# Performance work log

Hardware: AMD Instinct MI355X
Metric: run time of the kernel (lower is better)

Reference implementation:

```python
import jax, jax.numpy as jnp
import numpy as np

T, E, H, K = 8192, 512, 512, 19  # seq_len, embed_dim, per-direction hidden, tagset
START, STOP, NEG = 17, 18, -10000.0


def _lstm_dir(x, w_ih, w_hh, b_ih, b_hh, h0, c0):
    # x: [T, E]; PyTorch gate order i, f, g, o. Precompute input contribution.
    xg = x @ w_ih.T + b_ih + b_hh  # [T, 4H]

    def step(carry, xg_t):
        h, c = carry
        g = xg_t + h @ w_hh.T
        i, f, gg, o = jnp.split(g, 4)
        c = jax.nn.sigmoid(f) * c + jax.nn.sigmoid(i) * jnp.tanh(gg)
        h = jax.nn.sigmoid(o) * jnp.tanh(c)
        return (h, c), h

    _, hs = jax.lax.scan(step, (h0, c0), xg)
    return hs  # [T, H]


def setup_inputs() -> dict:
    key = jax.random.key(0)
    ks = jax.random.split(key, 16)
    s = 0.05
    trans = jax.random.normal(ks[13], (K, K), jnp.float32)
    trans = trans.at[START, :].set(NEG)  # never transition into START
    trans = trans.at[:, STOP].set(NEG)   # never transition from STOP
    return {
        "sentence": jax.random.normal(ks[0], (T, 1, E), jnp.float32),
        "w_ih_f": jax.random.normal(ks[1], (4 * H, E), jnp.float32) * s,
        "w_hh_f": jax.random.normal(ks[2], (4 * H, H), jnp.float32) * s,
        "b_ih_f": jax.random.normal(ks[3], (4 * H,), jnp.float32) * s,
        "b_hh_f": jax.random.normal(ks[4], (4 * H,), jnp.float32) * s,
        "w_ih_b": jax.random.normal(ks[5], (4 * H, E), jnp.float32) * s,
        "w_hh_b": jax.random.normal(ks[6], (4 * H, H), jnp.float32) * s,
        "b_ih_b": jax.random.normal(ks[7], (4 * H,), jnp.float32) * s,
        "b_hh_b": jax.random.normal(ks[8], (4 * H,), jnp.float32) * s,
        "h0": jax.random.normal(ks[9], (2, 1, H), jnp.float32),
        "c0": jax.random.normal(ks[10], (2, 1, H), jnp.float32),
        "W_tag": jax.random.normal(ks[11], (K, 2 * H), jnp.float32) * s,
        "b_tag": jax.random.normal(ks[12], (K,), jnp.float32) * s,
        "transitions": trans,
    }


def reference(sentence, w_ih_f, w_hh_f, b_ih_f, b_hh_f, w_ih_b, w_hh_b, b_ih_b, b_hh_b, h0, c0, W_tag, b_tag, transitions):
    x = sentence[:, 0, :]  # [T, E], batch = 1
    hs_f = _lstm_dir(x, w_ih_f, w_hh_f, b_ih_f, b_hh_f, h0[0, 0], c0[0, 0])
    hs_b = _lstm_dir(x[::-1], w_ih_b, w_hh_b, b_ih_b, b_hh_b, h0[1, 0], c0[1, 0])[::-1]
    lstm_out = jnp.concatenate([hs_f, hs_b], axis=-1)  # [T, 2H]
    feats = lstm_out @ W_tag.T + b_tag  # [T, K] emission scores

    # Viterbi decode: transitions[i, j] = score of j -> i
    init = jnp.full((K,), NEG, jnp.float32).at[START].set(0.0)

    def vstep(fv, feat):
        nt = fv[None, :] + transitions      # [K, K]
        bptr = jnp.argmax(nt, axis=1)       # best previous tag per current tag
        fv_new = jnp.max(nt, axis=1) + feat
        return fv_new, bptr

    fv, bptrs = jax.lax.scan(vstep, init, feats)  # bptrs: [T, K]
    terminal = fv + transitions[STOP]
    best = jnp.argmax(terminal)
    path_score = terminal[best]

    def back(tag, bptr):
        return bptr[tag], tag

    _, best_path = jax.lax.scan(back, best, bptrs, reverse=True)  # [T]
    return path_score, best_path
```

## Files before the change

kernel.cpp:

```cpp
#include <hip/hip_runtime.h>
#include <hip/hip_fp16.h>

#define T_LEN 8192
#define E_DIM 512
#define H_DIM 512
#define G4    2048
#define KTAGS 19
#define START_TAG 17
#define STOP_TAG  18
#define NEGV  (-10000.0f)
#define VCH   64
#define VCL   128
#define LSTM_LDS ((16384 + 256 + 1024 + 64) * 4)

typedef _Float16 h2v __attribute__((ext_vector_type(2)));
union HU { unsigned int u; h2v h; };

__device__ __forceinline__ float sigf_(float x) {
  x = fminf(fmaxf(x, -30.f), 30.f);
  return 1.f / (1.f + __expf(-x));
}
__device__ __forceinline__ float tanhf_(float x) {
  x = fminf(fmaxf(x, -15.f), 15.f);
  const float e = __expf(2.f * x);
  return (e - 1.f) / (e + 1.f);
}

__device__ __forceinline__ unsigned int pack2(float a, float b) {
  HU u; u.h.x = (_Float16)a; u.h.y = (_Float16)b; return u.u;
}

__device__ __forceinline__ float dot2f(unsigned int a, unsigned int b, float acc) {
#if __has_builtin(__builtin_amdgcn_fdot2)
  HU ua; ua.u = a; HU ub; ub.u = b;
  return __builtin_amdgcn_fdot2(ua.h, ub.h, acc, false);
#else
  HU ua; ua.u = a; HU ub; ub.u = b;
  return acc + (float)ua.h.x * (float)ub.h.x + (float)ua.h.y * (float)ub.h.y;
#endif
}

__global__ __launch_bounds__(256) void k_xg(
    const float* __restrict__ x,
    const float* __restrict__ wih_f, const float* __restrict__ bih_f, const float* __restrict__ bhh_f,
    const float* __restrict__ wih_b, const float* __restrict__ bih_b, const float* __restrict__ bhh_b,
    __half* __restrict__ xg_out)
{
  const int dir = blockIdx.z;
  const float* __restrict__ wih = dir ? wih_b : wih_f;
  const float* __restrict__ bih = dir ? bih_b : bih_f;
  const float* __restrict__ bhh = dir ? bhh_b : bhh_f;
  __shared__ float xs[16][68];
  __shared__ float wsd[16][68];
  const int tid = threadIdx.x;
  const int tm = tid >> 4, tn = tid & 15;
  const int m0 = blockIdx.y * 64, n0 = blockIdx.x * 64;
  const int lr = tid >> 2;
  const int lk = (tid & 3) << 2;
  float acc[4][4] = {{0.f,0.f,0.f,0.f},{0.f,0.f,0.f,0.f},{0.f,0.f,0.f,0.f},{0.f,0.f,0.f,0.f}};
  for (int k0 = 0; k0 < E_DIM; k0 += 16) {
    const int gm = m0 + lr;
    const int xrow = dir ? (T_LEN - 1 - gm) : gm;
    const float4 xa = *reinterpret_cast<const float4*>(&x[(size_t)xrow * E_DIM + k0 + lk]);
    const float4 wa = *reinterpret_cast<const float4*>(&wih[(size_t)(n0 + lr) * E_DIM + k0 + lk]);
    __syncthreads();
    xs[lk+0][lr] = xa.x; xs[lk+1][lr] = xa.y; xs[lk+2][lr] = xa.z; xs[lk+3][lr] = xa.w;
    wsd[lk+0][lr] = wa.x; wsd[lk+1][lr] = wa.y; wsd[lk+2][lr] = wa.z; wsd[lk+3][lr] = wa.w;
    __syncthreads();
    #pragma unroll
    for (int kk = 0; kk < 16; ++kk) {
      const float4 a = *reinterpret_cast<const float4*>(&xs[kk][tm << 2]);
      const float4 b = *reinterpret_cast<const float4*>(&wsd[kk][tn << 2]);
      acc[0][0] += a.x*b.x; acc[0][1] += a.x*b.y; acc[0][2] += a.x*b.z; acc[0][3] += a.x*b.w;
      acc[1][0] += a.y*b.x; acc[1][1] += a.y*b.y; acc[1][2] += a.y*b.z; acc[1][3] += a.y*b.w;
      acc[2][0] += a.z*b.x; acc[2][1] += a.z*b.y; acc[2][2] += a.z*b.z; acc[2][3] += a.z*b.w;
      acc[3][0] += a.w*b.x; acc[3][1] += a.w*b.y; acc[3][2] += a.w*b.z; acc[3][3] += a.w*b.w;
    }
  }
  const int n = n0 + (tn << 2);
  float4 bb;
  bb.x = bih[n+0] + bhh[n+0];
  bb.y = bih[n+1] + bhh[n+1];
  bb.z = bih[n+2] + bhh[n+2];
  bb.w = bih[n+3] + bhh[n+3];
  __half* o = xg_out + (size_t)dir * T_LEN * G4;
  #pragma unroll
  for (int mi = 0; mi < 4; ++mi) {
    const size_t base = (size_t)(m0 + (tm << 2) + mi) * G4 + n;
    unsigned int p0 = pack2(acc[mi][0] + bb.x, acc[mi][1] + bb.y);
    unsigned int p1 = pack2(acc[mi][2] + bb.z, acc[mi][3] + bb.w);
    uint2 st; st.x = p0; st.y = p1;
    *reinterpret_cast<uint2*>(&o[base]) = st;
  }
}

__global__ __launch_bounds__(512, 1) void k_lstm(
    const float* __restrict__ whh_f, const float* __restrict__ whh_b,
    const float* __restrict__ h0, const float* __restrict__ c0,
    const __half* __restrict__ xg_base, unsigned long long* __restrict__ hht)
{
  const int b = blockIdx.x;
  if ((b & 7) >= 2) return;
  const int dir = b & 7;
  const int idx = b >> 3;
  const float* __restrict__ whh = dir ? whh_b : whh_f;
  const __half* xg16 = xg_base + (size_t)dir * T_LEN * G4;
  unsigned long long* hp = hht + (size_t)dir * T_LEN * 256;

  extern __shared__ unsigned int lds[];
  unsigned int* wl  = lds;
  unsigned int* hlb = lds + 16384;
  float* pgl        = (float*)(lds + 16384 + 256);

  const int tid = threadIdx.x;
  const int w = tid >> 6, l = tid & 63;
  const int gate = l >> 4, j = l & 15;
  const int H0 = idx * 16;
  const int Rrow = gate * H_DIM + H0 + j;

  {
    const float4* src = reinterpret_cast<const float4*>(&whh[(size_t)Rrow * H_DIM + (w << 6)]);
    #pragma unroll
    for (int m = 0; m < 8; ++m) {
      const float4 a = src[2*m], d = src[2*m+1];
      uint4 pk;
      pk.x = pack2(a.x, a.y); pk.y = pack2(a.z, a.w);
      pk.z = pack2(d.x, d.y); pk.w = pack2(d.z, d.w);
      *reinterpret_cast<uint4*>(&wl[(((w << 3) + m) * 64 + l) * 4]) = pk;
    }
  }
  const uint4* wb = reinterpret_cast<const uint4*>(wl) + ((w << 3) * 64 + l);
  uint4 w0 = wb[0*64], w1 = wb[1*64], w2 = wb[2*64], w3 = wb[3*64],
        w4 = wb[4*64], w5 = wb[5*64], w6 = wb[6*64], w7 = wb[7*64];

  float cstate = 0.f;
  if (w == 0 && l < 16) cstate = c0[dir * H_DIM + H0 + l];
  float xcur = 0.f, xnext = 0.f;
  if (w == 0) {
    xcur  = __half2float(xg16[Rrow]);
    xnext = __half2float(xg16[(size_t)G4 + Rrow]);
  }

  for (int t = 0; t < T_LEN; ++t) {
    const int buf = t & 1;
    if (l < 32) {
      const int pw = (w << 5) + l;
      unsigned int pair;
      if (t > 0) {
        const unsigned long long* src = &hp[(size_t)(t - 1) * 256 + pw];
        unsigned long long v = __hip_atomic_load(src, __ATOMIC_RELAXED, __HIP_MEMORY_SCOPE_AGENT);
        while ((unsigned)(v >> 32) != (unsigned)t)
          v = __hip_atomic_load(src, __ATOMIC_RELAXED, __HIP_MEMORY_SCOPE_AGENT);
        pair = (unsigned)v;
      } else {
        pair = pack2(h0[dir * H_DIM + 2 * pw], h0[dir * H_DIM + 2 * pw + 1]);
      }
      hlb[pw] = pair;
    }
    const uint4* hb = reinterpret_cast<const uint4*>(&hlb[w << 5]);
    float acc0 = 0.f, acc1 = 0.f;
    uint4 hv;
    hv = hb[0];
    acc0 = dot2f(w0.x, hv.x, acc0); acc1 = dot2f(w0.y, hv.y, acc1);
    acc0 = dot2f(w0.z, hv.z, acc0); acc1 = dot2f(w0.w, hv.w, acc1);
    hv = hb[1];
    acc0 = dot2f(w1.x, hv.x, acc0); acc1 = dot2f(w1.y, hv.y, acc1);
    acc0 = dot2f(w1.z, hv.z, acc0); acc1 = dot2f(w1.w, hv.w, acc1);
    hv = hb[2];
    acc0 = dot2f(w2.x, hv.x, acc0); acc1 = dot2f(w2.y, hv.y, acc1);
    acc0 = dot2f(w2.z, hv.z, acc0); acc1 = dot2f(w2.w, hv.w, acc1);
    hv = hb[3];
    acc0 = dot2f(w3.x, hv.x, acc0); acc1 = dot2f(w3.y, hv.y, acc1);
    acc0 = dot2f(w3.z, hv.z, acc0); acc1 = dot2f(w3.w, hv.w, acc1);
    hv = hb[4];
    acc0 = dot2f(w4.x, hv.x, acc0); acc1 = dot2f(w4.y, hv.y, acc1);
    acc0 = dot2f(w4.z, hv.z, acc0); acc1 = dot2f(w4.w, hv.w, acc1);
    hv = hb[5];
    acc0 = dot2f(w5.x, hv.x, acc0); acc1 = dot2f(w5.y, hv.y, acc1);
    acc0 = dot2f(w5.z, hv.z, acc0); acc1 = dot2f(w5.w, hv.w, acc1);
    hv = hb[6];
    acc0 = dot2f(w6.x, hv.x, acc0); acc1 = dot2f(w6.y, hv.y, acc1);
    acc0 = dot2f(w6.z, hv.z, acc0); acc1 = dot2f(w6.w, hv.w, acc1);
    hv = hb[7];
    acc0 = dot2f(w7.x, hv.x, acc0); acc1 = dot2f(w7.y, hv.y, acc1);
    acc0 = dot2f(w7.z, hv.z, acc0); acc1 = dot2f(w7.w, hv.w, acc1);
    pgl[buf * 512 + (w << 6) + l] = acc0 + acc1;
    __syncthreads();

    if (w == 0) {
      const float* pb = &pgl[buf * 512 + l];
      const float tr = pb[0] + pb[64] + pb[128] + pb[192]
                     + pb[256] + pb[320] + pb[384] + pb[448];
      const float gv = tr + xcur;
      const bool isg = (gate == 2);
      const float sarg = isg ? 2.f * gv : gv;
      const float sg = sigf_(sarg);
      const float p = isg ? 2.f * sg - 1.f : sg;
      const float pi  = __shfl(p, j, 64);
      const float pf  = __shfl(p, 16 + j, 64);
      const float pgv = __shfl(p, 32 + j, 64);
      const float po  = __shfl(p, 48 + j, 64);
      float hval = 0.f;
      if (l < 16) {
        cstate = pf * cstate + pi * pgv;
        hval = po * tanhf_(cstate);
      }
      const float hop = __shfl(hval, l + 1, 64);
      if (l < 16 && (l & 1) == 0) {
        const unsigned long long pv =
            (unsigned long long)pack2(hval, hop) | ((unsigned long long)(t + 1) << 32);
        __hip_atomic_store(&hp[(size_t)t * 256 + idx * 8 + (l >> 1)], pv,
                           __ATOMIC_RELAXED, __HIP_MEMORY_SCOPE_AGENT);
      }
      xcur = xnext;
      xnext = (t + 2 < T_LEN) ? __half2float(xg16[(size_t)(t + 2) * G4 + Rrow]) : 0.f;
    }
  }
}

__global__ __launch_bounds__(64) void k_feats(
    const unsigned long long* __restrict__ hht, const float* __restrict__ Wtag,
    const float* __restrict__ btag, float* __restrict__ feats)
{
  const int t = blockIdx.x;
  const int tid = threadIdx.x;
  __shared__ float hbuf[1024];
  const unsigned long long* hfp = hht + (size_t)t * 256;
  const unsigned long long* hbp = hht + (size_t)T_LEN * 256 + (size_t)(T_LEN - 1 - t) * 256;
  for (int m = tid; m < 256; m += 64) {
    HU u; u.u = (unsigned)hfp[m];
    hbuf[2*m] = (float)u.h.x; hbuf[2*m+1] = (float)u.h.y;
    HU v; v.u = (unsigned)hbp[m];
    hbuf[512 + 2*m] = (float)v.h.x; hbuf[512 + 2*m+1] = (float)v.h.y;
  }
  __syncthreads();
  const int k = tid;
  if (k >= KTAGS) return;
  const float* wr = &Wtag[(size_t)k * 1024];
  float acc = btag[k];
  #pragma unroll 4
  for (int d = 0; d < 256; ++d) {
    const float4 h4 = *reinterpret_cast<const float4*>(&hbuf[4 * d]);
    const float4 w4 = *reinterpret_cast<const float4*>(&wr[4 * d]);
    acc += h4.x*w4.x + h4.y*w4.y + h4.z*w4.z + h4.w*w4.w;
  }
  feats[(size_t)t * KTAGS + k] = acc;
}

__global__ __launch_bounds__(384) void k_vit1(
    const float* __restrict__ feats, const float* __restrict__ trans,
    float* __restrict__ Mc)
{
  const int cidx = blockIdx.x;
  const int tid = threadIdx.x;
  const bool act = tid < KTAGS * KTAGS;
  const int i = tid / KTAGS, j = tid % KTAGS;
  __shared__ float M[2][KTAGS * KTAGS];
  __shared__ float ft[KTAGS];
  float trow[KTAGS];
  if (act) {
    #pragma unroll
    for (int kk = 0; kk < KTAGS; ++kk) trow[kk] = trans[i * KTAGS + kk];
  }
  const int s = cidx * VCL;
  if (tid < KTAGS) ft[tid] = feats[(size_t)s * KTAGS + tid];
  __syncthreads();
  if (act) M[0][tid] = trow[j] + ft[i];
  for (int u = 1; u < VCL; ++u) {
    __syncthreads();
    if (tid < KTAGS) ft[tid] = feats[(size_t)(s + u) * KTAGS + tid];
    __syncthreads();
    const float* Mr = M[(u + 1) & 1];
    if (act) {
      float m = -3.4e38f;
      #pragma unroll
      for (int kk = 0; kk < KTAGS; ++kk)
        m = fmaxf(m, trow[kk] + Mr[kk * KTAGS + j]);
      M[u & 1][tid] = m + ft[i];
    }
  }
  __syncthreads();
  if (act) Mc[(size_t)cidx * (KTAGS * KTAGS) + tid] = M[(VCL - 1) & 1][tid];
}

__global__ __launch_bounds__(64) void k_vit2(
    const float* __restrict__ Mc, const float* __restrict__ trans,
    float* __restrict__ fvs, float* __restrict__ d_out, int* __restrict__ best)
{
  const int l = threadIdx.x;
  const bool act = l < KTAGS;
  float fv = act ? ((l == START_TAG) ? 0.f : NEGV) : -3.4e38f;
  for (int cidx = 0; cidx < VCH; ++cidx) {
    if (act) fvs[cidx * KTAGS + l] = fv;
    const float* Mr = &Mc[(size_t)cidx * (KTAGS * KTAGS) + (act ? l : 0) * KTAGS];
    float m = -3.4e38f;
    #pragma unroll
    for (int jj = 0; jj < KTAGS; ++jj) {
      const float fvj = __shfl(fv, jj, 64);
      m = fmaxf(m, Mr[jj] + fvj);
    }
    fv = act ? m : -3.4e38f;
  }
  const float trs = act ? trans[STOP_TAG * KTAGS + l] : 0.f;
  float tv = act ? (fv + trs) : -3.4e38f;
  int bi = l;
  #pragma unroll
  for (int off = 1; off < 64; off <<= 1) {
    const float ov = __shfl_xor(tv, off, 64);
    const int oi = __shfl_xor(bi, off, 64);
    if (ov > tv || (ov == tv && oi < bi)) { tv = ov; bi = oi; }
  }
  if (l == 0) { d_out[0] = tv; *best = bi; }
}

__global__ __launch_bounds__(64) void k_vit3(
    const float* __restrict__ feats, const float* __restrict__ trans,
    const float* __restrict__ fvs, unsigned char* __restrict__ bptr)
{
  const int cidx = blockIdx.x;
  const int l = threadIdx.x;
  const bool act = l < KTAGS;
  float trow[KTAGS];
  #pragma unroll
  for (int jj = 0; jj < KTAGS; ++jj)
    trow[jj] = act ? trans[l * KTAGS + jj] : NEGV;
  float fv = act ? fvs[cidx * KTAGS + l] : -3.4e38f;
  const int s = cidx * VCL;
  for (int u = 0; u < VCL; ++u) {
    const int tt = s + u;
    const float fcur = act ? feats[(size_t)tt * KTAGS + l] : 0.f;
    float v[KTAGS];
    #pragma unroll
    for (int jj = 0; jj < KTAGS; ++jj)
      v[jj] = __shfl(fv, jj, 64) + trow[jj];
    float a[10];
    #pragma unroll
    for (int q = 0; q < 9; ++q) a[q] = fmaxf(v[2*q], v[2*q+1]);
    a[9] = v[18];
    const float mv = fmaxf(fmaxf(fmaxf(fmaxf(a[0],a[1]), fmaxf(a[2],a[3])),
                                 fmaxf(fmaxf(a[4],a[5]), fmaxf(a[6],a[7]))), fmaxf(a[8],a[9]));
    unsigned bits = 0u;
    #pragma unroll
    for (int jj = 0; jj < KTAGS; ++jj)
      bits |= (v[jj] == mv) ? (1u << jj) : 0u;
    const int am = __ffs(bits) - 1;
    fv = mv + fcur;
    if (act) bptr[(size_t)tt * KTAGS + l] = (unsigned char)am;
  }
}

__global__ __launch_bounds__(64) void k_chunkF(
    const unsigned char* __restrict__ bptr, unsigned char* __restrict__ F)
{
  const int cidx = blockIdx.x;
  const int g = threadIdx.x;
  if (g >= KTAGS) return;
  const int e = (cidx + 1) * 128 - 1, s = cidx * 128;
  int tag = g;
  for (int t = e; t >= s; --t) tag = bptr[(size_t)t * KTAGS + tag];
  F[cidx * KTAGS + g] = (unsigned char)tag;
}

__global__ void k_bounds(const unsigned char* __restrict__ F,
                         const int* __restrict__ best, int* __restrict__ boundary)
{
  if (threadIdx.x != 0 || blockIdx.x != 0) return;
  int tag = *best;
  boundary[63] = tag;
  for (int cidx = 63; cidx >= 1; --cidx) {
    tag = F[cidx * KTAGS + tag];
    boundary[cidx - 1] = tag;
  }
}

__global__ __launch_bounds__(64) void k_path(
    const unsigned char* __restrict__ bptr, const int* __restrict__ boundary,
    float* __restrict__ d_out)
{
  const int cidx = blockIdx.x;
  if (threadIdx.x != 0) return;
  const int e = (cidx + 1) * 128 - 1, s = cidx * 128;
  int tag = boundary[cidx];
  d_out[1 + e] = (float)tag;
  for (int t = e - 1; t >= s; --t) {
    tag = bptr[(size_t)(t + 1) * KTAGS + tag];
    d_out[1 + t] = (float)tag;
  }
}

extern "C" void kernel_launch(void* const* d_in, const int* in_sizes, int n_in,
                              void* d_out, int out_size, void* d_ws, size_t ws_size,
                              hipStream_t stream) {
  (void)in_sizes; (void)n_in; (void)out_size; (void)ws_size;
  const float* x      = (const float*)d_in[0];
  const float* wih_f  = (const float*)d_in[1];
  const float* whh_f  = (const float*)d_in[2];
  const float* bih_f  = (const float*)d_in[3];
  const float* bhh_f  = (const float*)d_in[4];
  const float* wih_b  = (const float*)d_in[5];
  const float* whh_b  = (const float*)d_in[6];
  const float* bih_b  = (const float*)d_in[7];
  const float* bhh_b  = (const float*)d_in[8];
  const float* h0     = (const float*)d_in[9];
  const float* c0     = (const float*)d_in[10];
  const float* Wtag   = (const float*)d_in[11];
  const float* btag   = (const float*)d_in[12];
  const float* trans  = (const float*)d_in[13];
  float* out = (float*)d_out;
  char* ws = (char*)d_ws;

  size_t off = 0;
  auto alloc = [&](size_t bytes) -> void* {
    void* p = ws + off;
    off += (bytes + 255) & ~(size_t)255;
    return p;
  };
  __half* xg              = (__half*)alloc((size_t)2 * T_LEN * G4 * 2);
  unsigned long long* hht = (unsigned long long*)alloc((size_t)2 * T_LEN * 256 * 8);
  float* feats            = (float*)alloc((size_t)T_LEN * KTAGS * 4);
  unsigned char* bptr     = (unsigned char*)alloc((size_t)T_LEN * KTAGS);
  float* Mc               = (float*)alloc((size_t)VCH * KTAGS * KTAGS * 4);
  float* fvs              = (float*)alloc((size_t)VCH * KTAGS * 4);
  unsigned char* F        = (unsigned char*)alloc(VCH * KTAGS);
  int* boundary           = (int*)alloc(VCH * 4);
  int* best               = (int*)alloc(4);


  hipFuncSetAttribute(reinterpret_cast<const void*>(k_lstm),
                      hipFuncAttributeMaxDynamicSharedMemorySize, LSTM_LDS);

  const dim3 gx(G4 / 64, T_LEN / 64, 2);
  k_xg<<<gx, 256, 0, stream>>>(x, wih_f, bih_f, bhh_f, wih_b, bih_b, bhh_b, xg);
  k_lstm<<<256, 512, LSTM_LDS, stream>>>(whh_f, whh_b, h0, c0, xg, hht);
  k_feats<<<T_LEN, 64, 0, stream>>>(hht, Wtag, btag, feats);
  k_vit1<<<VCH, 384, 0, stream>>>(feats, trans, Mc);
  k_vit2<<<1, 64, 0, stream>>>(Mc, trans, fvs, out, best);
  k_vit3<<<VCH, 64, 0, stream>>>(feats, trans, fvs, bptr);
  k_chunkF<<<VCH, 64, 0, stream>>>(bptr, F);
  k_bounds<<<1, 64, 0, stream>>>(F, best, boundary);
  k_path<<<VCH, 64, 0, stream>>>(bptr, boundary, out);
}
```

Measured before the change: 8.613 ms.

## Distribute LSTM gate reduction and cell update across all eight waves

Before, wave 0 alone summed the eight partial dot products per gate row and computed all 16 hidden outputs. Now each wave reduces its own 2 hidden units with cross-lane shuffles over a padded LDS buffer and publishes one packed pair. This is meant to shorten the serial post-barrier tail of each recurrent step, and the padding of the partial-sum buffer aims to avoid LDS bank conflicts. The cost is that every wave now does shuffle reductions, and the input-gate prefetch is issued inside the loop only one step ahead.

```diff
diff --git a/kernel.cpp b/kernel.cpp
--- a/kernel.cpp
+++ b/kernel.cpp
@@ -11,7 +11,7 @@
 #define NEGV  (-10000.0f)
 #define VCH   64
 #define VCL   128
-#define LSTM_LDS ((16384 + 256 + 1024 + 64) * 4)
+#define LSTM_LDS ((16384 + 256 + 1040 + 64) * 4)
 
 typedef _Float16 h2v __attribute__((ext_vector_type(2)));
 union HU { unsigned int u; h2v h; };
@@ -118,6 +118,9 @@
   const int H0 = idx * 16;
   const int Rrow = gate * H_DIM + H0 + j;
 
+  const int q = l & 7;
+  const int RrowE = (q >> 1) * H_DIM + H0 + (w << 1) + (q & 1);
+
   {
     const float4* src = reinterpret_cast<const float4*>(&whh[(size_t)Rrow * H_DIM + (w << 6)]);
     #pragma unroll
@@ -134,12 +137,9 @@
         w4 = wb[4*64], w5 = wb[5*64], w6 = wb[6*64], w7 = wb[7*64];
 
   float cstate = 0.f;
-  if (w == 0 && l < 16) cstate = c0[dir * H_DIM + H0 + l];
-  float xcur = 0.f, xnext = 0.f;
-  if (w == 0) {
-    xcur  = __half2float(xg16[Rrow]);
-    xnext = __half2float(xg16[(size_t)G4 + Rrow]);
-  }
+  if (l < 2) cstate = c0[dir * H_DIM + H0 + (w << 1) + l];
+  float xcur = 0.f;
+  if (l < 8) xcur = __half2float(xg16[RrowE]);
 
   for (int t = 0; t < T_LEN; ++t) {
     const int buf = t & 1;
@@ -157,6 +157,10 @@
       }
       hlb[pw] = pair;
     }
+    float xnext = 0.f;
+    if (l < 8 && t + 1 < T_LEN)
+      xnext = __half2float(xg16[(size_t)(t + 1) * G4 + RrowE]);
+
     const uint4* hb = reinterpret_cast<const uint4*>(&hlb[w << 5]);
     float acc0 = 0.f, acc1 = 0.f;
     uint4 hv;
@@ -184,37 +188,39 @@
     hv = hb[7];
     acc0 = dot2f(w7.x, hv.x, acc0); acc1 = dot2f(w7.y, hv.y, acc1);
     acc0 = dot2f(w7.z, hv.z, acc0); acc1 = dot2f(w7.w, hv.w, acc1);
-    pgl[buf * 512 + (w << 6) + l] = acc0 + acc1;
+    pgl[buf * 520 + w * 65 + l] = acc0 + acc1;
     __syncthreads();
 
-    if (w == 0) {
-      const float* pb = &pgl[buf * 512 + l];
-      const float tr = pb[0] + pb[64] + pb[128] + pb[192]
-                     + pb[256] + pb[320] + pb[384] + pb[448];
+    {
+      const int cw = l >> 3;
+      const int r_e = ((q >> 1) << 4) + (w << 1) + (q & 1);
+      float tr = pgl[buf * 520 + cw * 65 + r_e];
+      tr += __shfl_xor(tr, 8, 64);
+      tr += __shfl_xor(tr, 16, 64);
+      tr += __shfl_xor(tr, 32, 64);
       const float gv = tr + xcur;
-      const bool isg = (gate == 2);
+      const bool isg = ((q >> 1) == 2);
       const float sarg = isg ? 2.f * gv : gv;
       const float sg = sigf_(sarg);
       const float p = isg ? 2.f * sg - 1.f : sg;
-      const float pi  = __shfl(p, j, 64);
-      const float pf  = __shfl(p, 16 + j, 64);
-      const float pgv = __shfl(p, 32 + j, 64);
-      const float po  = __shfl(p, 48 + j, 64);
+      const float pi  = __shfl(p, (l & 1), 64);
+      const float pf  = __shfl(p, 2 + (l & 1), 64);
+      const float pgv = __shfl(p, 4 + (l & 1), 64);
+      const float po  = __shfl(p, 6 + (l & 1), 64);
       float hval = 0.f;
-      if (l < 16) {
+      if (l < 2) {
         cstate = pf * cstate + pi * pgv;
         hval = po * tanhf_(cstate);
       }
-      const float hop = __shfl(hval, l + 1, 64);
-      if (l < 16 && (l & 1) == 0) {
+      const float hop = __shfl(hval, 1, 64);
+      if (l == 0) {
         const unsigned long long pv =
             (unsigned long long)pack2(hval, hop) | ((unsigned long long)(t + 1) << 32);
-        __hip_atomic_store(&hp[(size_t)t * 256 + idx * 8 + (l >> 1)], pv,
+        __hip_atomic_store(&hp[(size_t)t * 256 + idx * 8 + w], pv,
                            __ATOMIC_RELAXED, __HIP_MEMORY_SCOPE_AGENT);
       }
-      xcur = xnext;
-      xnext = (t + 2 < T_LEN) ? __half2float(xg16[(size_t)(t + 2) * G4 + Rrow]) : 0.f;
-    }
+    }
+    xcur = xnext;
   }
 }
 
```

New measurement: 12.39 ms. +43.9%, slower.
